# Kernel tuning notes

Hardware: AMD Instinct MI355X
Metric: run time of the kernel (lower is better)

Reference implementation:

```python
import jax, jax.numpy as jnp
import numpy as np

M_TOKENS, D_IN, D_OUT = 4096, 4096, 16384


def setup_inputs() -> dict:
    key = jax.random.key(0)
    k1, k2, k3, k4 = jax.random.split(key, 4)
    x = jax.random.normal(k1, (M_TOKENS, D_IN), dtype=jnp.float32)
    # pre-quantized int8 weight, stored [K, N] as in qweight_kn
    qweight_kn = jax.random.randint(k2, (D_IN, D_OUT), -127, 128, dtype=jnp.int8)
    # per-output-channel weight dequant scales (float16 buffer, used as fp32 in kernel)
    weight_scales = jax.random.uniform(k3, (D_OUT,), dtype=jnp.float32, minval=1e-3, maxval=2e-2)
    bias = jax.random.normal(k4, (D_OUT,), dtype=jnp.float32) * 0.01
    return {"x": x, "qweight_kn": qweight_kn, "weight_scales": weight_scales, "bias": bias}


def reference(x, qweight_kn, weight_scales, bias):
    target_dtype = x.dtype
    x2 = x.reshape(-1, x.shape[-1])  # [M, K]
    # dynamic per-token (per-row) symmetric quantization
    x_max = jnp.max(jnp.abs(x2), axis=-1, keepdims=True).astype(jnp.float32) + 1e-5
    x_scales = x_max / 127.0  # [M, 1]
    x_int8 = jnp.clip(jnp.round(x2.astype(jnp.float32) / x_scales), -128, 127).astype(jnp.int8)
    acc = jax.lax.dot_general(
        x_int8, qweight_kn,
        dimension_numbers=(((1,), (0,)), ((), ())),
        preferred_element_type=jnp.int32,
    )  # [M, N] int32
    # fused dequant: row act-scale * col weight-scale, plus bias
    c = acc.astype(jnp.float32) * x_scales * weight_scales[None, :].astype(jnp.float32)
    c = c + bias[None, :]
    out = c.astype(jnp.bfloat16)  # kernel stores bf16
    return out.reshape(*x.shape[:-1], -1).astype(target_dtype)
```

## Files before the change

### kernel.cpp

```cpp
#include <hip/hip_runtime.h>
#include <hip/hip_bf16.h>
#include <stdint.h>

typedef int v4i __attribute__((ext_vector_type(4)));

#define GM 4096
#define GN 16384
#define GK 4096
#define BM 256
#define BN 256
#define BK 64
#define NT (GK / BK)

__device__ __forceinline__ void gload16(const void* g, void* l) {
  __builtin_amdgcn_global_load_lds(
      (const __attribute__((address_space(1))) void*)g,
      (__attribute__((address_space(3))) void*)l, 16, 0, 0);
}

__global__ __launch_bounds__(256) void quant_rows(
    const float* __restrict__ x, int8_t* __restrict__ xq2,
    float* __restrict__ xs, int K) {
  const int row = blockIdx.x;
  const int t = threadIdx.x;
  const float4* src = (const float4*)(x + (size_t)row * K) + t * 4;
  float4 v[4];
  float m = 0.f;
#pragma unroll
  for (int i = 0; i < 4; ++i) {
    v[i] = src[i];
    m = fmaxf(m, fmaxf(fmaxf(fabsf(v[i].x), fabsf(v[i].y)),
                       fmaxf(fabsf(v[i].z), fabsf(v[i].w))));
  }
#pragma unroll
  for (int off = 1; off < 64; off <<= 1)
    m = fmaxf(m, __shfl_xor(m, off, 64));
  __shared__ float wmax[4];
  if ((t & 63) == 0) wmax[t >> 6] = m;
  __syncthreads();
  const float gm = fmaxf(fmaxf(wmax[0], wmax[1]), fmaxf(wmax[2], wmax[3]));
  const float scale = (gm + 1e-5f) / 127.0f;
  if (t == 0) xs[row] = scale;
  unsigned packed[4];
#pragma unroll
  for (int i = 0; i < 4; ++i) {
    float fv[4] = {v[i].x, v[i].y, v[i].z, v[i].w};
    unsigned p = 0;
#pragma unroll
    for (int j = 0; j < 4; ++j) {
      int q = (int)rintf(fv[j] / scale);
      q = max(-128, min(127, q));
      p |= (unsigned)(q & 0xff) << (8 * j);
    }
    packed[i] = p;
  }
  const int tm = row >> 8, f = (row >> 4) & 15, fr = row & 15;
  const int kt = t >> 2, kg = t & 3;
  int8_t* dst =
      xq2 + ((((size_t)(tm * 64 + kt) * 16 + f) * 64) + fr + 16 * kg) * 16;
  *(int4*)dst =
      make_int4((int)packed[0], (int)packed[1], (int)packed[2], (int)packed[3]);
}

__global__ __launch_bounds__(256) void transpose_pack(
    const int* __restrict__ W32, int8_t* __restrict__ Wt2, int K, int N) {
  __shared__ __align__(16) int8_t tile[64][80];
  const int t = threadIdx.x;
  const int n0 = blockIdx.x * 64;
  const int k0 = blockIdx.y * 64;
  const int ln = t & 63;
  const int wv = t >> 6;
#pragma unroll
  for (int it = 0; it < 16; ++it) {
    const int kk = wv * 16 + it;
    tile[ln][kk] = (int8_t)W32[(size_t)(k0 + kk) * N + n0 + ln];
  }
  __syncthreads();
  const int lane = ln;
  const int4 v = *(const int4*)&tile[wv * 16 + (lane & 15)][(lane >> 4) * 16];
  const int tn = n0 >> 8;
  const int kt = k0 >> 6;
  const int f = ((n0 >> 4) & 15) + wv;
  *(int4*)(Wt2 + (((size_t)(tn * 64 + kt) * 16 + f) * 64 + lane) * 16) = v;
}

__global__ __launch_bounds__(512, 2) void gemm_i8(
    const int8_t* __restrict__ Xq2, const int8_t* __restrict__ Wt2,
    const float* __restrict__ xs, const float* __restrict__ wsc,
    const float* __restrict__ bias, float* __restrict__ C) {
  __shared__ __align__(16) int8_t lA[4][16384];

  const int t = threadIdx.x;
  const int lane = t & 63;
  const int w = t >> 6;
  const int wr = w >> 2;
  const int wc = w & 3;
  const int fr = lane & 15;
  const int kg = lane >> 4;

  const int bid = blockIdx.x;
  const int xcd = bid & 7;
  const int q = bid >> 3;
  const int tm = q & 15;
  const int tn = xcd * 8 + (q >> 4);
  const size_t rowA0 = (size_t)tm * BM;
  const size_t rowB0 = (size_t)tn * BN;

  const int8_t* aqB = Xq2 + (size_t)tm * 1048576 + w * 2048 + (size_t)lane * 16;
  const int dstO = w * 2048;

#define STAGE(KT, SLOT)                                           \
  {                                                               \
    const int8_t* p = aqB + (size_t)(KT)*16384;                   \
    gload16(p, &lA[(SLOT)][0] + dstO);                            \
    gload16(p + 1024, &lA[(SLOT)][0] + dstO + 1024);              \
  }

  const int8_t* bq = Wt2 + (size_t)tn * 1048576 + wc * 4096 + (size_t)lane * 16;

  v4i acc[8][4] = {};
  v4i areg[8], breg[4][4];

#define LD(dst, ptr)                                        \
  asm volatile("global_load_dwordx4 %0, %1, off"            \
               : "=v"(dst)                                  \
               : "v"(ptr)                                   \
               : "memory")

#define LOADB(KT, S)                                        \
  {                                                         \
    const int8_t* bp = bq + (size_t)(KT)*16384;             \
    LD(breg[S][0], bp);                                     \
    LD(breg[S][1], bp + 1024);                              \
    LD(breg[S][2], bp + 2048);                              \
    LD(breg[S][3], bp + 3072);                              \
  }

#define RD_A(MI, SLOT)                                                     \
  areg[MI] = *(const v4i*)&lA[(SLOT)][(wr * 8 + (MI)) * 1024 + lane * 16];

#define SB __builtin_amdgcn_sched_barrier(0)

#define BODY(T, SLOT)                                                         \
  {                                                                           \
                  \
    asm volatile("s_waitcnt vmcnt(12)" ::: "memory");                         \
    __builtin_amdgcn_s_barrier();  \
    SB;                                                                       \
    STAGE(((T) + 3) & (NT - 1), ((SLOT) + 3) & 3);                            \
    LOADB(((T) + 3) & (NT - 1), ((SLOT) + 3) & 3);                            \
    SB;                                                                       \
    RD_A(0, SLOT); RD_A(1, SLOT); RD_A(2, SLOT); RD_A(3, SLOT);               \
    SB;                                                                       \
    RD_A(4, SLOT); RD_A(5, SLOT); RD_A(6, SLOT); RD_A(7, SLOT);               \
    SB;                                                                       \
    asm volatile("s_waitcnt lgkmcnt(4)" ::: "memory");        \
    SB;                                                                       \
    __builtin_amdgcn_s_setprio(1);                                            \
    _Pragma("unroll") for (int mi = 0; mi < 4; ++mi)                          \
        _Pragma("unroll") for (int nj = 0; nj < 4; ++nj)                      \
            acc[mi][nj] = __builtin_amdgcn_mfma_i32_16x16x64_i8(              \
                areg[mi], breg[SLOT][nj], acc[mi][nj], 0, 0, 0);              \
    __builtin_amdgcn_s_setprio(0);                                            \
    asm volatile("s_waitcnt lgkmcnt(0)" ::: "memory");        \
    SB;                                                                       \
    __builtin_amdgcn_s_setprio(1);                                            \
    _Pragma("unroll") for (int mi = 4; mi < 8; ++mi)                          \
        _Pragma("unroll") for (int nj = 0; nj < 4; ++nj)                      \
            acc[mi][nj] = __builtin_amdgcn_mfma_i32_16x16x64_i8(              \
                areg[mi], breg[SLOT][nj], acc[mi][nj], 0, 0, 0);              \
    __builtin_amdgcn_s_setprio(0);                                            \
  }

  STAGE(0, 0);
  LOADB(0, 0);
  STAGE(1, 1);
  LOADB(1, 1);
  STAGE(2, 2);
  LOADB(2, 2);

  for (int kt = 0; kt < NT; kt += 4) {
    BODY(kt, 0);
    BODY(kt + 1, 1);
    BODY(kt + 2, 2);
    BODY(kt + 3, 3);
  }
  asm volatile("s_waitcnt vmcnt(0) lgkmcnt(0)" ::: "memory");
  SB;

#pragma unroll
  for (int nj = 0; nj < 4; ++nj) {
    const int col_l = wc * 64 + nj * 16 + fr;
    const float wsv = wsc[rowB0 + col_l];
    const float bv = bias[rowB0 + col_l];
#pragma unroll
    for (int mi = 0; mi < 8; ++mi) {
#pragma unroll
      for (int r = 0; r < 4; ++r) {
        const size_t row = rowA0 + wr * 128 + mi * 16 + kg * 4 + r;
        const float f = (float)acc[mi][nj][r] * xs[row] * wsv + bv;
        C[row * GN + rowB0 + col_l] = __bfloat162float(__float2bfloat16(f));
      }
    }
  }
}

extern "C" void kernel_launch(void* const* d_in, const int* in_sizes, int n_in,
                              void* d_out, int out_size, void* d_ws, size_t ws_size,
                              hipStream_t stream) {
  const int M = GM, K = GK, N = GN;
  const float* x = (const float*)d_in[0];
  const int* W32 = (const int*)d_in[1];
  const float* wsc = (const float*)d_in[2];
  const float* bias = (const float*)d_in[3];
  float* out = (float*)d_out;

  float* xs = (float*)d_ws;
  int8_t* Xq2 = (int8_t*)d_ws + 16384;
  int8_t* Wt2 = (int8_t*)d_ws + 16384 + (size_t)M * K;

  transpose_pack<<<dim3(N / 64, K / 64), 256, 0, stream>>>(W32, Wt2, K, N);
  quant_rows<<<M, 256, 0, stream>>>(x, Xq2, xs, K);
  gemm_i8<<<dim3((M / BM) * (N / BN)), 512, 0, stream>>>(Xq2, Wt2, xs, wsc, bias,
                                                         out);
}
```

Before: 431.8 us.

## Give each wave a private double-buffered LDS A tile and drop block barriers

```diff
diff --git a/kernel.cpp b/kernel.cpp
--- a/kernel.cpp
+++ b/kernel.cpp
@@ -88,7 +88,7 @@
     const int8_t* __restrict__ Xq2, const int8_t* __restrict__ Wt2,
     const float* __restrict__ xs, const float* __restrict__ wsc,
     const float* __restrict__ bias, float* __restrict__ C) {
-  __shared__ __align__(16) int8_t lA[4][16384];
+  __shared__ __align__(16) int8_t lA[8][2][8192];
 
   const int t = threadIdx.x;
   const int lane = t & 63;
@@ -106,20 +106,14 @@
   const size_t rowA0 = (size_t)tm * BM;
   const size_t rowB0 = (size_t)tn * BN;
 
-  const int8_t* aqB = Xq2 + (size_t)tm * 1048576 + w * 2048 + (size_t)lane * 16;
-  const int dstO = w * 2048;
-
-#define STAGE(KT, SLOT)                                           \
-  {                                                               \
-    const int8_t* p = aqB + (size_t)(KT)*16384;                   \
-    gload16(p, &lA[(SLOT)][0] + dstO);                            \
-    gload16(p + 1024, &lA[(SLOT)][0] + dstO + 1024);              \
-  }
+  const int8_t* aqB =
+      Xq2 + (size_t)tm * 1048576 + wr * 8192 + (size_t)lane * 16;
+  int8_t* lw = &lA[w][0][0];
 
   const int8_t* bq = Wt2 + (size_t)tn * 1048576 + wc * 4096 + (size_t)lane * 16;
 
   v4i acc[8][4] = {};
-  v4i areg[8], breg[4][4];
+  v4i areg[8], breg[2][4];
 
 #define LD(dst, ptr)                                        \
   asm volatile("global_load_dwordx4 %0, %1, off"            \
@@ -127,32 +121,39 @@
                : "v"(ptr)                                   \
                : "memory")
 
-#define LOADB(KT, S)                                        \
+#define ISSUE(T, S)                                         \
   {                                                         \
-    const int8_t* bp = bq + (size_t)(KT)*16384;             \
+    const int8_t* ap = aqB + (size_t)(T)*16384;             \
+    int8_t* lp = lw + (S)*8192;                             \
+    gload16(ap, lp);                                        \
+    gload16(ap + 1024, lp + 1024);                          \
+    gload16(ap + 2048, lp + 2048);                          \
+    gload16(ap + 3072, lp + 3072);                          \
+    gload16(ap + 4096, lp + 4096);                          \
+    gload16(ap + 5120, lp + 5120);                          \
+    gload16(ap + 6144, lp + 6144);                          \
+    gload16(ap + 7168, lp + 7168);                          \
+    const int8_t* bp = bq + (size_t)(T)*16384;              \
     LD(breg[S][0], bp);                                     \
     LD(breg[S][1], bp + 1024);                              \
     LD(breg[S][2], bp + 2048);                              \
     LD(breg[S][3], bp + 3072);                              \
   }
 
-#define RD_A(MI, SLOT)                                                     \
-  areg[MI] = *(const v4i*)&lA[(SLOT)][(wr * 8 + (MI)) * 1024 + lane * 16];
+#define RD_A(MI, S)                                         \
+  areg[MI] = *(const v4i*)(lw + (S)*8192 + (MI)*1024 + lane * 16);
 
 #define SB __builtin_amdgcn_sched_barrier(0)
 
-#define BODY(T, SLOT)                                                         \
+#define BODY(T, S)                                                            \
   {                                                                           \
-                  \
-    asm volatile("s_waitcnt vmcnt(12)" ::: "memory");                         \
-    __builtin_amdgcn_s_barrier();  \
-    SB;                                                                       \
-    STAGE(((T) + 3) & (NT - 1), ((SLOT) + 3) & 3);                            \
-    LOADB(((T) + 3) & (NT - 1), ((SLOT) + 3) & 3);                            \
-    SB;                                                                       \
-    RD_A(0, SLOT); RD_A(1, SLOT); RD_A(2, SLOT); RD_A(3, SLOT);               \
-    SB;                                                                       \
-    RD_A(4, SLOT); RD_A(5, SLOT); RD_A(6, SLOT); RD_A(7, SLOT);               \
+    ISSUE(((T) + 1) & (NT - 1), (S) ^ 1);   \
+    SB;                                       \
+    asm volatile("s_waitcnt vmcnt(12)" ::: "memory");     \
+    SB;                                                                       \
+    RD_A(0, S); RD_A(1, S); RD_A(2, S); RD_A(3, S);                           \
+    SB;                                                                       \
+    RD_A(4, S); RD_A(5, S); RD_A(6, S); RD_A(7, S);                           \
     SB;                                                                       \
     asm volatile("s_waitcnt lgkmcnt(4)" ::: "memory");        \
     SB;                                                                       \
@@ -160,7 +161,7 @@
     _Pragma("unroll") for (int mi = 0; mi < 4; ++mi)                          \
         _Pragma("unroll") for (int nj = 0; nj < 4; ++nj)                      \
             acc[mi][nj] = __builtin_amdgcn_mfma_i32_16x16x64_i8(              \
-                areg[mi], breg[SLOT][nj], acc[mi][nj], 0, 0, 0);              \
+                areg[mi], breg[S][nj], acc[mi][nj], 0, 0, 0);                 \
     __builtin_amdgcn_s_setprio(0);                                            \
     asm volatile("s_waitcnt lgkmcnt(0)" ::: "memory");        \
     SB;                                                                       \
@@ -168,22 +169,15 @@
     _Pragma("unroll") for (int mi = 4; mi < 8; ++mi)                          \
         _Pragma("unroll") for (int nj = 0; nj < 4; ++nj)                      \
             acc[mi][nj] = __builtin_amdgcn_mfma_i32_16x16x64_i8(              \
-                areg[mi], breg[SLOT][nj], acc[mi][nj], 0, 0, 0);              \
+                areg[mi], breg[S][nj], acc[mi][nj], 0, 0, 0);                 \
     __builtin_amdgcn_s_setprio(0);                                            \
   }
 
-  STAGE(0, 0);
-  LOADB(0, 0);
-  STAGE(1, 1);
-  LOADB(1, 1);
-  STAGE(2, 2);
-  LOADB(2, 2);
-
-  for (int kt = 0; kt < NT; kt += 4) {
+  ISSUE(0, 0);
+
+  for (int kt = 0; kt < NT; kt += 2) {
     BODY(kt, 0);
     BODY(kt + 1, 1);
-    BODY(kt + 2, 2);
-    BODY(kt + 3, 3);
   }
   asm volatile("s_waitcnt vmcnt(0) lgkmcnt(0)" ::: "memory");
   SB;
```

Result: slower. 482.1 us (+11.6%).
